# Kernel tuning notes

Measured on AMD Instinct MI355X. Metric: run time of the kernel, lower is better.

## Reference

```python
import jax, jax.numpy as jnp
import numpy as np
from jax.ops import segment_sum

N_NODES = 100000
N_EDGES = 1600000
HIDDEN = 128


def gcn_conv(x, src, dst, w, W, b, num_nodes):
    """PyG GCNConv: add self-loops (weight 1), symmetric deg^-1/2 normalization,
    gather from src, scatter-add to dst. x: [N, Fin], W: [Fin, Fout]."""
    loop = jnp.arange(num_nodes, dtype=src.dtype)
    s = jnp.concatenate([src, loop])
    d = jnp.concatenate([dst, loop])
    ww = jnp.concatenate([w, jnp.ones((num_nodes,), dtype=w.dtype)])
    deg = segment_sum(ww, d, num_segments=num_nodes)           # [N]
    dis = jnp.where(deg > 0, jax.lax.rsqrt(jnp.where(deg > 0, deg, 1.0)), 0.0)
    norm = dis[s] * ww * dis[d]                                # [E+N]
    h = x @ W                                                  # [N, Fout]
    msg = norm[:, None] * h[s]                                 # [E+N, Fout]
    out = segment_sum(msg, d, num_segments=num_nodes)          # [N, Fout]
    return out + b


def setup_inputs() -> dict:
    key = jax.random.key(0)
    ks = jax.random.split(key, 12)
    h = HIDDEN
    sc = lambda fan_in: 1.0 / np.sqrt(fan_in)
    return {
        "x": jax.random.normal(ks[0], (N_NODES, 1), dtype=jnp.float32),
        "edge_index": jax.random.randint(ks[1], (2, N_EDGES), 0, N_NODES, dtype=jnp.int64),
        "edge_weight": jax.random.uniform(ks[2], (N_EDGES,), dtype=jnp.float32),
        "W1": jax.random.normal(ks[3], (1, h), dtype=jnp.float32) * sc(1),
        "b1": jnp.zeros((h,), dtype=jnp.float32),
        "W2": jax.random.normal(ks[4], (h, 2 * h), dtype=jnp.float32) * sc(h),
        "b2": jnp.zeros((2 * h,), dtype=jnp.float32),
        "Wl1": jax.random.normal(ks[5], (2 * h, h), dtype=jnp.float32) * sc(2 * h),
        "bl1": jnp.zeros((h,), dtype=jnp.float32),
        "Wl2": jax.random.normal(ks[6], (h, 1), dtype=jnp.float32) * sc(h),
        "bl2": jnp.zeros((1,), dtype=jnp.float32),
    }


def reference(x, edge_index, edge_weight, W1, b1, W2, b2, Wl1, bl1, Wl2, bl2):
    n = x.shape[0]
    src, dst = edge_index[0], edge_index[1]
    h = jax.nn.relu(gcn_conv(x, src, dst, edge_weight, W1, b1, n))
    h = jax.nn.relu(gcn_conv(h, src, dst, edge_weight, W2, b2, n))
    h = jax.nn.relu(h @ Wl1 + bl1)
    return h @ Wl2 + bl2
```

## Files before the change

kernel.cpp:

```cpp
#include <hip/hip_runtime.h>


#define HD 128
#define HD2 256
#define BSHIFT 8
#define BNODES 256
#define SRCBITS 17

typedef __attribute__((ext_vector_type(8))) short bf8_t;
typedef __attribute__((ext_vector_type(4))) float f32x4;

static inline size_t align256(size_t x) { return (x + 255) & ~(size_t)255; }

__device__ inline ushort f2bf(float f) {
    uint u = __float_as_uint(f);
    uint r = u + 0x7fffu + ((u >> 16) & 1u);
    return (ushort)(r >> 16);
}
__device__ inline uint packbf(float a, float b) {
    return (uint)f2bf(a) | ((uint)f2bf(b) << 16);
}

__global__ void k_init(const float* __restrict__ W2, const float* __restrict__ Wl1,
                       ushort* __restrict__ Bt1, ushort* __restrict__ Bt2,
                       int* __restrict__ bfill) {
    int o = blockIdx.x * blockDim.x + threadIdx.x;
    if (o < 512) bfill[o] = 0;
    if (o >= 32768) return;
    {
        int k0 = o & 7, n = (o >> 3) & 255, k8 = o >> 11;
        Bt1[o] = f2bf(W2[(size_t)(k8 * 8 + k0) * 256 + n]);
    }
    {
        int k0 = o & 7, n = (o >> 3) & 127, k8 = o >> 10;
        Bt2[o] = f2bf(Wl1[(size_t)(k8 * 8 + k0) * 128 + n]);
    }
}

__global__ __launch_bounds__(256) void k_part(const int* __restrict__ ei,
                                              const float* __restrict__ ew,
                                              int* __restrict__ bfill,
                                              uint2* __restrict__ stg,
                                              int E, int nbuck, int cap) {
    __shared__ int lcnt[4][512];
    __shared__ int lbase[4][512];
    int tid = threadIdx.x;
    int wvid = tid >> 6;
    for (int i = tid; i < nbuck; i += 256) {
        lcnt[0][i] = 0; lcnt[1][i] = 0; lcnt[2][i] = 0; lcnt[3][i] = 0;
    }
    __syncthreads();
    bool is64 = (ei[1] == 0) && (ei[3] == 0) && (ei[5] == 0) && (ei[7] == 0);
    int e0 = blockIdx.x * 2048;
    uint pack[8]; uint wb[8]; int bkt[8]; int rank[8];
    for (int u = 0; u < 8; u++) {
        int e = e0 + u * 256 + tid;
        bkt[u] = -1;
        if (e < E) {
            int s, d;
            if (is64) { s = ei[2 * e]; d = ei[2 * (E + e)]; }
            else      { s = ei[e];     d = ei[E + e]; }
            bkt[u] = d >> BSHIFT;
            pack[u] = ((uint)(d & (BNODES - 1)) << SRCBITS) | (uint)s;
            wb[u] = __float_as_uint(ew[e]);
            rank[u] = atomicAdd(&lcnt[wvid][bkt[u]], 1);
        }
    }
    __syncthreads();
    for (int i = tid; i < nbuck; i += 256) {
        int t0 = lcnt[0][i], t1 = lcnt[1][i], t2 = lcnt[2][i], t3 = lcnt[3][i];
        int tot = t0 + t1 + t2 + t3;
        int base = tot ? atomicAdd(&bfill[i], tot) : 0;
        lbase[0][i] = base;
        lbase[1][i] = base + t0;
        lbase[2][i] = base + t0 + t1;
        lbase[3][i] = base + t0 + t1 + t2;
    }
    __syncthreads();
    for (int u = 0; u < 8; u++)
        if (bkt[u] >= 0)
            stg[(size_t)bkt[u] * cap + lbase[wvid][bkt[u]] + rank[u]] =
                make_uint2(pack[u], wb[u]);
}

__global__ __launch_bounds__(512) void k_fine(const uint2* __restrict__ stg,
                                              const int* __restrict__ bfill,
                                              const float* __restrict__ x,
                                              float* __restrict__ dis,
                                              float* __restrict__ p,
                                              int* __restrict__ rowptr,
                                              int2* __restrict__ cv,
                                              int cap, int N, int E, int nbuck) {
    __shared__ int cnt_l[BNODES];
    __shared__ int base_l[BNODES];
    __shared__ float degf[BNODES];
    __shared__ int wsum[8];
    int b = blockIdx.x, tid = threadIdx.x;
    int lane = tid & 63, wvid = tid >> 6;
    int a = (tid < b && tid < nbuck) ? bfill[tid] : 0;
    for (int off = 32; off > 0; off >>= 1) a += __shfl_xor(a, off);
    if (lane == 0) wsum[wvid] = a;
    __syncthreads();
    int cb = wsum[0] + wsum[1] + wsum[2] + wsum[3] +
             wsum[4] + wsum[5] + wsum[6] + wsum[7];
    int n = bfill[b];
    if (b == nbuck - 1 && tid == 0) rowptr[N] = E;
    const uint2* s = stg + (size_t)b * cap;
    if (tid < BNODES) { cnt_l[tid] = 0; degf[tid] = 1.0f; }
    __syncthreads();
    for (int i = tid; i < n; i += 512)
        atomicAdd(&cnt_l[s[i].x >> SRCBITS], 1);
    __syncthreads();
    int c = 0;
    if (tid < BNODES) { c = cnt_l[tid]; cnt_l[tid] = 0; }
    int v = c;
    for (int off = 1; off < 64; off <<= 1) {
        int u = __shfl_up(v, off);
        if (lane >= off) v += u;
    }
    if (wvid < 4 && lane == 63) wsum[wvid] = v;
    __syncthreads();
    if (tid < BNODES) {
        int wpre = 0;
        for (int k = 0; k < wvid; k++) wpre += wsum[k];
        base_l[tid] = v + wpre - c;
    }
    __syncthreads();
    for (int i = tid; i < n; i += 512) {
        uint2 r = s[i];
        int dl = r.x >> SRCBITS;
        int src = (int)(r.x & ((1u << SRCBITS) - 1));
        int pos = cb + base_l[dl] + atomicAdd(&cnt_l[dl], 1);
        cv[pos] = make_int2(src, (int)r.y);
        atomicAdd(&degf[dl], __uint_as_float(r.y));
    }
    __syncthreads();
    int gid = (b << BSHIFT) + tid;
    if (tid < BNODES && gid < N) {
        rowptr[gid] = cb + base_l[tid];
        float r = rsqrtf(degf[tid]);
        dis[gid] = r;
        p[gid] = r * x[gid];
    }
}

__global__ __launch_bounds__(256) void k_q(const int* __restrict__ rowptr,
                                           const int2* __restrict__ cv,
                                           const float* __restrict__ dis,
                                           const float* __restrict__ p,
                                           float2* __restrict__ tp, int N) {
    int gid = blockIdx.x * blockDim.x + threadIdx.x;
    int wid = gid >> 4;
    int sl = threadIdx.x & 15;
    if (wid >= N) return;
    int beg = rowptr[wid], end = rowptr[wid + 1];
    float s = 0.0f;
    for (int i = beg + sl; i < end; i += 16) {
        int2 pr = cv[i];
        s += __int_as_float(pr.y) * p[pr.x];
    }
    s += __shfl_xor(s, 1);
    s += __shfl_xor(s, 2);
    s += __shfl_xor(s, 4);
    s += __shfl_xor(s, 8);
    if (sl == 0) {
        float r = dis[wid];
        tp[wid] = make_float2(r * (s + p[wid]), r);
    }
}

__global__ __launch_bounds__(256) void k_agg(const int* __restrict__ rowptr,
                                             const int2* __restrict__ cv,
                                             const float2* __restrict__ tp,
                                             const float* __restrict__ W1,
                                             const float* __restrict__ b1,
                                             uint* __restrict__ z, int N) {
    __shared__ float2 eb[4][64];
    int tid = threadIdx.x;
    int wvid = tid >> 6, lane = tid & 63;
    int half = lane >> 5, hl = lane & 31;
    int node = ((blockIdx.x * 256 + tid) >> 6) * 2 + half;
    bool valid = node < N;
    float4 w1 = valid ? *(const float4*)(W1 + hl * 4) : make_float4(0, 0, 0, 0);
    float4 bb = valid ? *(const float4*)(b1 + hl * 4) : make_float4(0, 0, 0, 0);
    int beg = 0, end = 0;
    if (valid) { beg = rowptr[node]; end = rowptr[node + 1]; }
    int nb = (end - beg + 31) >> 5;
    nb = max(nb, __shfl_xor(nb, 32));
    float4 aA = make_float4(0, 0, 0, 0), aB = make_float4(0, 0, 0, 0);
    const float4* ebp = (const float4*)&eb[wvid][half * 32];
    for (int bt = 0; bt < nb; bt++) {
        int eidx = beg + bt * 32 + hl;
        float wd = 0.0f, tt = 0.0f;
        if (eidx < end) {
            int2 pr = cv[eidx];
            float2 tps = tp[pr.x];
            wd = __int_as_float(pr.y) * tps.y;
            tt = tps.x;
        }
        eb[wvid][lane] = make_float2(wd, tt);
        int m = min(32, end - (beg + bt * 32)); if (m < 0) m = 0;
        int hm = (m + 1) >> 1;
        hm = max(hm, __shfl_xor(hm, 32));
        int u = 0;
        for (; u + 2 <= hm; u += 2) {
            float4 e2 = ebp[u];
            float4 e3 = ebp[u + 1];
            aA.x = fmaf(e2.x, fmaxf(fmaf(e2.y, w1.x, bb.x), 0.f), aA.x);
            aA.y = fmaf(e2.x, fmaxf(fmaf(e2.y, w1.y, bb.y), 0.f), aA.y);
            aA.z = fmaf(e2.x, fmaxf(fmaf(e2.y, w1.z, bb.z), 0.f), aA.z);
            aA.w = fmaf(e2.x, fmaxf(fmaf(e2.y, w1.w, bb.w), 0.f), aA.w);
            aA.x = fmaf(e2.z, fmaxf(fmaf(e2.w, w1.x, bb.x), 0.f), aA.x);
            aA.y = fmaf(e2.z, fmaxf(fmaf(e2.w, w1.y, bb.y), 0.f), aA.y);
            aA.z = fmaf(e2.z, fmaxf(fmaf(e2.w, w1.z, bb.z), 0.f), aA.z);
            aA.w = fmaf(e2.z, fmaxf(fmaf(e2.w, w1.w, bb.w), 0.f), aA.w);
            aB.x = fmaf(e3.x, fmaxf(fmaf(e3.y, w1.x, bb.x), 0.f), aB.x);
            aB.y = fmaf(e3.x, fmaxf(fmaf(e3.y, w1.y, bb.y), 0.f), aB.y);
            aB.z = fmaf(e3.x, fmaxf(fmaf(e3.y, w1.z, bb.z), 0.f), aB.z);
            aB.w = fmaf(e3.x, fmaxf(fmaf(e3.y, w1.w, bb.w), 0.f), aB.w);
            aB.x = fmaf(e3.z, fmaxf(fmaf(e3.w, w1.x, bb.x), 0.f), aB.x);
            aB.y = fmaf(e3.z, fmaxf(fmaf(e3.w, w1.y, bb.y), 0.f), aB.y);
            aB.z = fmaf(e3.z, fmaxf(fmaf(e3.w, w1.z, bb.z), 0.f), aB.z);
            aB.w = fmaf(e3.z, fmaxf(fmaf(e3.w, w1.w, bb.w), 0.f), aB.w);
        }
        if (u < hm) {
            float4 e2 = ebp[u];
            aA.x = fmaf(e2.x, fmaxf(fmaf(e2.y, w1.x, bb.x), 0.f), aA.x);
            aA.y = fmaf(e2.x, fmaxf(fmaf(e2.y, w1.y, bb.y), 0.f), aA.y);
            aA.z = fmaf(e2.x, fmaxf(fmaf(e2.y, w1.z, bb.z), 0.f), aA.z);
            aA.w = fmaf(e2.x, fmaxf(fmaf(e2.y, w1.w, bb.w), 0.f), aA.w);
            aA.x = fmaf(e2.z, fmaxf(fmaf(e2.w, w1.x, bb.x), 0.f), aA.x);
            aA.y = fmaf(e2.z, fmaxf(fmaf(e2.w, w1.y, bb.y), 0.f), aA.y);
            aA.z = fmaf(e2.z, fmaxf(fmaf(e2.w, w1.z, bb.z), 0.f), aA.z);
            aA.w = fmaf(e2.z, fmaxf(fmaf(e2.w, w1.w, bb.w), 0.f), aA.w);
        }
    }
    if (!valid) return;
    float2 tpd = tp[node];
    float rd = tpd.y;
    float o0 = rd * (aA.x + aB.x + rd * fmaxf(fmaf(tpd.x, w1.x, bb.x), 0.f));
    float o1 = rd * (aA.y + aB.y + rd * fmaxf(fmaf(tpd.x, w1.y, bb.y), 0.f));
    float o2 = rd * (aA.z + aB.z + rd * fmaxf(fmaf(tpd.x, w1.z, bb.z), 0.f));
    float o3 = rd * (aA.w + aB.w + rd * fmaxf(fmaf(tpd.x, w1.w, bb.w), 0.f));
    ((uint2*)(z + (size_t)node * 64))[hl] = make_uint2(packbf(o0, o1), packbf(o2, o3));
}

__global__ __launch_bounds__(256) void k_mlp(const ushort* __restrict__ A,
                                             const ushort* __restrict__ Bt1,
                                             const ushort* __restrict__ Bt2,
                                             const float* __restrict__ b2,
                                             const float* __restrict__ bl1,
                                             const float* __restrict__ wl2,
                                             const float* __restrict__ bl2,
                                             float* __restrict__ out, int M) {
    __shared__ ushort st[4][32][40];
    int tid = threadIdx.x;
    int wv = tid >> 6, lane = tid & 63;
    int l15 = lane & 15, quad = lane >> 4;
    int row0 = blockIdx.x * 128 + wv * 32;
    int r0 = row0 + l15;      r0 = r0 < M ? r0 : M - 1;
    int r1 = row0 + 16 + l15; r1 = r1 < M ? r1 : M - 1;

    bf8_t a1[2][4];
    for (int kc = 0; kc < 4; kc++) {
        a1[0][kc] = *(const bf8_t*)(A + (size_t)r0 * 128 + kc * 32 + quad * 8);
        a1[1][kc] = *(const bf8_t*)(A + (size_t)r1 * 128 + kc * 32 + quad * 8);
    }
    f32x4 acc2[2][8];
    for (int i = 0; i < 2; i++)
        for (int j = 0; j < 8; j++) acc2[i][j] = (f32x4){0.f, 0.f, 0.f, 0.f};

    for (int c = 0; c < 8; c++) {
        f32x4 acc1[2][2];
        for (int i = 0; i < 2; i++)
            for (int j = 0; j < 2; j++) acc1[i][j] = (f32x4){0.f, 0.f, 0.f, 0.f};
        for (int kc = 0; kc < 4; kc++)
            for (int nt = 0; nt < 2; nt++) {
                bf8_t b = *(const bf8_t*)(Bt1 +
                    ((size_t)(kc * 4 + quad) * 256 + c * 32 + nt * 16 + l15) * 8);
                acc1[0][nt] = __builtin_amdgcn_mfma_f32_16x16x32_bf16(a1[0][kc], b, acc1[0][nt], 0, 0, 0);
                acc1[1][nt] = __builtin_amdgcn_mfma_f32_16x16x32_bf16(a1[1][kc], b, acc1[1][nt], 0, 0, 0);
            }
        for (int nt = 0; nt < 2; nt++) {
            float bb = b2[c * 32 + nt * 16 + l15];
            for (int mt = 0; mt < 2; mt++)
                for (int rg = 0; rg < 4; rg++)
                    st[wv][mt * 16 + quad * 4 + rg][nt * 16 + l15] =
                        f2bf(fmaxf(acc1[mt][nt][rg] + bb, 0.f));
        }
        bf8_t a2_0 = *(const bf8_t*)&st[wv][l15][quad * 8];
        bf8_t a2_1 = *(const bf8_t*)&st[wv][16 + l15][quad * 8];
        for (int nt2 = 0; nt2 < 8; nt2++) {
            bf8_t b = *(const bf8_t*)(Bt2 +
                ((size_t)(c * 4 + quad) * 128 + nt2 * 16 + l15) * 8);
            acc2[0][nt2] = __builtin_amdgcn_mfma_f32_16x16x32_bf16(a2_0, b, acc2[0][nt2], 0, 0, 0);
            acc2[1][nt2] = __builtin_amdgcn_mfma_f32_16x16x32_bf16(a2_1, b, acc2[1][nt2], 0, 0, 0);
        }
    }
    float rs[2][4] = {};
    for (int nt2 = 0; nt2 < 8; nt2++) {
        int col = nt2 * 16 + l15;
        float bb = bl1[col], ww = wl2[col];
        for (int mt = 0; mt < 2; mt++)
            for (int rg = 0; rg < 4; rg++)
                rs[mt][rg] += fmaxf(acc2[mt][nt2][rg] + bb, 0.f) * ww;
    }
    float base = bl2[0];
    for (int mt = 0; mt < 2; mt++)
        for (int rg = 0; rg < 4; rg++) {
            float s = rs[mt][rg];
            s += __shfl_xor(s, 1);
            s += __shfl_xor(s, 2);
            s += __shfl_xor(s, 4);
            s += __shfl_xor(s, 8);
            int row = row0 + mt * 16 + quad * 4 + rg;
            if (l15 == 0 && row < M) out[row] = s + base;
        }
}

extern "C" void kernel_launch(void* const* d_in, const int* in_sizes, int n_in,
                              void* d_out, int out_size, void* d_ws, size_t ws_size,
                              hipStream_t stream) {
    const float* x   = (const float*)d_in[0];
    const int*   ei  = (const int*)d_in[1];
    const float* ew  = (const float*)d_in[2];
    const float* W1  = (const float*)d_in[3];
    const float* b1  = (const float*)d_in[4];
    const float* W2  = (const float*)d_in[5];
    const float* b2  = (const float*)d_in[6];
    const float* Wl1 = (const float*)d_in[7];
    const float* bl1 = (const float*)d_in[8];
    const float* Wl2 = (const float*)d_in[9];
    const float* bl2 = (const float*)d_in[10];
    float* out = (float*)d_out;
    const int N = in_sizes[0];
    const int E = in_sizes[2];

    const int nbuck = (N + BNODES - 1) >> BSHIFT;
    const int cap = ((E / nbuck) * 5) / 4 + 1024;

    char* w = (char*)d_ws;
    size_t off = 0;
    auto alloc = [&](size_t bytes) -> void* {
        void* p = w + off;
        off = align256(off + bytes);
        return p;
    };
    uint*   z      = (uint*)alloc((size_t)N * 64 * 4);
    float2* tp     = (float2*)alloc((size_t)N * 8);
    float*  dis    = (float*)alloc((size_t)N * 4);
    float*  p_     = (float*)alloc((size_t)N * 4);
    int*    rowptr = (int*)alloc((size_t)(N + 1) * 4);
    int2*   cv     = (int2*)alloc((size_t)E * 8);
    uint2*  stg    = (uint2*)alloc((size_t)nbuck * cap * 8);
    int*    bfill  = (int*)alloc(512 * 4);
    ushort* Bt1    = (ushort*)alloc(32768 * 2);
    ushort* Bt2    = (ushort*)alloc(32768 * 2);

    k_init<<<128, 256, 0, stream>>>(W2, Wl1, Bt1, Bt2, bfill);
    k_part<<<(E + 2047) / 2048, 256, 0, stream>>>(ei, ew, bfill, stg, E, nbuck, cap);
    k_fine<<<nbuck, 512, 0, stream>>>(stg, bfill, x, dis, p_, rowptr, cv, cap, N, E, nbuck);
    k_q<<<(N * 16 + 255) / 256, 256, 0, stream>>>(rowptr, cv, dis, p_, tp, N);
    k_agg<<<(N + 7) / 8, 256, 0, stream>>>(rowptr, cv, tp, W1, b1, z, N);
    k_mlp<<<(N + 127) / 128, 256, 0, stream>>>((const ushort*)z, Bt1, Bt2,
                                               b2, bl1, Wl2, bl2, out, N);
}
```

Baseline: 207.7 us.

## Stage partitioned edges in LDS sorted by bucket before global scatter

The bucket partition kernel now processes 4096 edges per block and computes a block-local exclusive scan over bucket counts. It sorts the packed edge records into shared memory by bucket, then writes them out in bucket-contiguous order so neighbouring threads hit neighbouring global addresses. This replaces the random per-edge scatter with more coalesced stores, at the cost of about 48KB of extra LDS per block, lower occupancy, fewer blocks and additional scans and barriers. The bucket capacity is also rounded to a multiple of 8.

```diff
diff --git a/kernel.cpp b/kernel.cpp
--- a/kernel.cpp
+++ b/kernel.cpp
@@ -6,6 +6,7 @@
 #define BSHIFT 8
 #define BNODES 256
 #define SRCBITS 17
+#define EPB 4096
 
 typedef __attribute__((ext_vector_type(8))) short bf8_t;
 typedef __attribute__((ext_vector_type(4))) float f32x4;
@@ -44,43 +45,82 @@
                                               int E, int nbuck, int cap) {
     __shared__ int lcnt[4][512];
     __shared__ int lbase[4][512];
+    __shared__ int lpre[512];
+    __shared__ int delta[512];
+    __shared__ uint2 sstage[EPB];
+    __shared__ uint  ga[EPB];
+    __shared__ int wscan[8];
+    __shared__ int nvs;
     int tid = threadIdx.x;
-    int wvid = tid >> 6;
-    for (int i = tid; i < nbuck; i += 256) {
+    int wvid = tid >> 6, lane = tid & 63;
+    for (int i = tid; i < 512; i += 256) {
         lcnt[0][i] = 0; lcnt[1][i] = 0; lcnt[2][i] = 0; lcnt[3][i] = 0;
     }
     __syncthreads();
     bool is64 = (ei[1] == 0) && (ei[3] == 0) && (ei[5] == 0) && (ei[7] == 0);
-    int e0 = blockIdx.x * 2048;
-    uint pack[8]; uint wb[8]; int bkt[8]; int rank[8];
-    for (int u = 0; u < 8; u++) {
+    int e0 = blockIdx.x * EPB;
+    uint pack[16]; uint wb[16]; short bkt[16]; short rank[16];
+    for (int u = 0; u < 16; u++) {
         int e = e0 + u * 256 + tid;
         bkt[u] = -1;
         if (e < E) {
             int s, d;
             if (is64) { s = ei[2 * e]; d = ei[2 * (E + e)]; }
             else      { s = ei[e];     d = ei[E + e]; }
-            bkt[u] = d >> BSHIFT;
+            bkt[u] = (short)(d >> BSHIFT);
             pack[u] = ((uint)(d & (BNODES - 1)) << SRCBITS) | (uint)s;
             wb[u] = __float_as_uint(ew[e]);
-            rank[u] = atomicAdd(&lcnt[wvid][bkt[u]], 1);
-        }
-    }
-    __syncthreads();
-    for (int i = tid; i < nbuck; i += 256) {
+            rank[u] = (short)atomicAdd(&lcnt[wvid][bkt[u]], 1);
+        }
+    }
+    __syncthreads();
+    for (int i = tid; i < 512; i += 256) {
         int t0 = lcnt[0][i], t1 = lcnt[1][i], t2 = lcnt[2][i], t3 = lcnt[3][i];
-        int tot = t0 + t1 + t2 + t3;
-        int base = tot ? atomicAdd(&bfill[i], tot) : 0;
-        lbase[0][i] = base;
-        lbase[1][i] = base + t0;
-        lbase[2][i] = base + t0 + t1;
-        lbase[3][i] = base + t0 + t1 + t2;
-    }
-    __syncthreads();
-    for (int u = 0; u < 8; u++)
-        if (bkt[u] >= 0)
-            stg[(size_t)bkt[u] * cap + lbase[wvid][bkt[u]] + rank[u]] =
-                make_uint2(pack[u], wb[u]);
+        lbase[0][i] = 0; lbase[1][i] = t0;
+        lbase[2][i] = t0 + t1; lbase[3][i] = t0 + t1 + t2;
+        lcnt[0][i] = t0 + t1 + t2 + t3;
+    }
+    __syncthreads();
+    int inc[2];
+    for (int r = 0; r < 2; r++) {
+        int v = lcnt[0][r * 256 + tid];
+        for (int off = 1; off < 64; off <<= 1) {
+            int u = __shfl_up(v, off);
+            if (lane >= off) v += u;
+        }
+        inc[r] = v;
+        if (lane == 63) wscan[r * 4 + wvid] = v;
+    }
+    __syncthreads();
+    if (tid == 0) {
+        int run = 0;
+        for (int s2 = 0; s2 < 8; s2++) { int t = wscan[s2]; wscan[s2] = run; run += t; }
+        nvs = run;
+    }
+    __syncthreads();
+    for (int r = 0; r < 2; r++) {
+        int i = r * 256 + tid;
+        int tot = lcnt[0][i];
+        int excl = inc[r] - tot + wscan[r * 4 + wvid];
+        int gb = 0;
+        if (tot && i < nbuck) gb = atomicAdd(&bfill[i], tot);
+        lpre[i] = excl;
+        delta[i] = i * cap + gb - excl;
+    }
+    __syncthreads();
+    for (int u = 0; u < 16; u++)
+        if (bkt[u] >= 0) {
+            int b = bkt[u];
+            int loc = lpre[b] + lbase[wvid][b] + rank[u];
+            sstage[loc] = make_uint2(pack[u], wb[u]);
+            ga[loc] = (uint)(delta[b] + loc);
+        }
+    __syncthreads();
+    int nv = nvs;
+    for (int ch = 0; ch < 16; ch++) {
+        int loc = ch * 256 + tid;
+        if (loc < nv) stg[ga[loc]] = sstage[loc];
+    }
 }
 
 __global__ __launch_bounds__(512) void k_fine(const uint2* __restrict__ stg,
@@ -337,7 +377,7 @@
     const int E = in_sizes[2];
 
     const int nbuck = (N + BNODES - 1) >> BSHIFT;
-    const int cap = ((E / nbuck) * 5) / 4 + 1024;
+    const int cap = ((((E / nbuck) * 5) / 4 + 1024) + 7) & ~7;
 
     char* w = (char*)d_ws;
     size_t off = 0;
@@ -358,7 +398,7 @@
     ushort* Bt2    = (ushort*)alloc(32768 * 2);
 
     k_init<<<128, 256, 0, stream>>>(W2, Wl1, Bt1, Bt2, bfill);
-    k_part<<<(E + 2047) / 2048, 256, 0, stream>>>(ei, ew, bfill, stg, E, nbuck, cap);
+    k_part<<<(E + EPB - 1) / EPB, 256, 0, stream>>>(ei, ew, bfill, stg, E, nbuck, cap);
     k_fine<<<nbuck, 512, 0, stream>>>(stg, bfill, x, dis, p_, rowptr, cv, cap, N, E, nbuck);
     k_q<<<(N * 16 + 255) / 256, 256, 0, stream>>>(rowptr, cv, dis, p_, tp, N);
     k_agg<<<(N + 7) / 8, 256, 0, stream>>>(rowptr, cv, tp, W1, b1, z, N);
```

New measurement: 195.6 us. 5.8% less time.
